# Performance work log

Measured on AMD Instinct MI355X. Metric: run time of the kernel, lower is better.

## Reference

```python
import jax, jax.numpy as jnp
import numpy as np

EPS = 1e-5
MODES = 64
KERNEL = 25
PRED = 336
N_ENC = 2

def rmsnorm(x, w):
    return x * jax.lax.rsqrt(jnp.mean(jnp.square(x), axis=-1, keepdims=True) + EPS) * w

def ffn(x, w1, b1, w2, b2):
    return jax.nn.gelu(x @ w1 + b1, approximate=False) @ w2 + b2

def series_decomp(x):
    # moving average with zero padding (Conv1d, kernel=KERNEL, weight=1/KERNEL)
    pad = (KERNEL - 1) // 2
    xp = jnp.pad(x, ((0, 0), (pad, pad), (0, 0)))
    cs = jnp.cumsum(xp, axis=1)
    cs = jnp.concatenate([jnp.zeros_like(cs[:, :1]), cs], axis=1)
    t = (cs[:, KERNEL:, :] - cs[:, :-KERNEL, :]) / KERNEL  # [B,T,C]
    return x - t, t

def fourier_block(x, w, nw):
    # x: [B,T,C]; w: [MODES,C,2] learned complex weights; nw: [C] rms scale
    B, T, C = x.shape
    Xf = jnp.fft.rfft(x, axis=1)                      # [B,F,C] complex64
    mag = jnp.sum(Xf[:, 1:].real**2 + Xf[:, 1:].imag**2, axis=-1)  # [B,F-1]
    K = min(MODES, Xf.shape[1] - 1)
    _, idx = jax.lax.top_k(mag, K)
    idx = idx + 1                                      # skip DC, [B,K]
    Xsel = jnp.take_along_axis(Xf, idx[:, :, None], axis=1)  # [B,K,C]
    Wc = w[:K, :, 0] + 1j * w[:K, :, 1]               # [K,C]
    Ysel = Xsel * Wc[None]                             # [B,K,C]
    Yf = jnp.zeros_like(Xf).at[jnp.arange(B)[:, None], idx].set(Ysel)
    y = jnp.fft.irfft(Yf, n=T, axis=1)                 # [B,T,C]
    return rmsnorm(y, nw)

def setup_inputs() -> dict:
    key = jax.random.key(0)
    ks = iter(jax.random.split(key, 64))
    B, L, Cin, Cout, D, FF = 32, 1024, 8, 8, 512, 2048
    r = lambda *s: jax.random.normal(next(ks), s, dtype=jnp.float32) * 0.02
    z = lambda *s: jnp.zeros(s, dtype=jnp.float32)
    o = lambda *s: jnp.ones(s, dtype=jnp.float32)
    return {
        'x': jax.random.normal(next(ks), (B, L, Cin), dtype=jnp.float32),
        'enc_in_w': r(Cin, D), 'enc_in_b': z(D),
        'dec_in_w': r(Cin, D), 'dec_in_b': z(D),
        'enc_freq_w': r(N_ENC, MODES, D, 2), 'enc_freq_nw': o(N_ENC, D),
        'enc_n1': o(N_ENC, D), 'enc_n2': o(N_ENC, D),
        'enc_w1': r(N_ENC, D, FF), 'enc_b1': z(N_ENC, FF),
        'enc_w2': r(N_ENC, FF, D), 'enc_b2': z(N_ENC, D),
        'dec_freq_w': r(MODES, D, 2), 'dec_freq_nw': o(D),
        'dec_n1': o(D), 'dec_n2': o(D), 'dec_nx': o(D),
        'dec_cross_w': r(D, D), 'dec_cross_b': z(D),
        'dec_w1': r(D, FF), 'dec_b1': z(FF),
        'dec_w2': r(FF, D), 'dec_b2': z(D),
        'seas_w': r(D, Cout), 'seas_b': z(Cout),
        'tr_w1': r(D, FF), 'tr_b1': z(FF),
        'tr_w2': r(FF, Cout), 'tr_b2': z(Cout),
        'mix_w': r(Cout, Cout), 'mix_b': z(Cout),
        'qpos': jax.random.normal(next(ks), (1, PRED, D), dtype=jnp.float32) * 0.02,
    }

def reference(x, enc_in_w, enc_in_b, dec_in_w, dec_in_b,
              enc_freq_w, enc_freq_nw, enc_n1, enc_n2, enc_w1, enc_b1, enc_w2, enc_b2,
              dec_freq_w, dec_freq_nw, dec_n1, dec_n2, dec_nx, dec_cross_w, dec_cross_b,
              dec_w1, dec_b1, dec_w2, dec_b2, seas_w, seas_b,
              tr_w1, tr_b1, tr_w2, tr_b2, mix_w, mix_b, qpos):
    s, t = series_decomp(x)
    sez = s @ enc_in_w + enc_in_b                      # [B,L,D]
    for i in range(N_ENC):
        sez = sez + fourier_block(rmsnorm(sez, enc_n1[i]), enc_freq_w[i], enc_freq_nw[i])
        sez = sez + ffn(rmsnorm(sez, enc_n2[i]), enc_w1[i], enc_b1[i], enc_w2[i], enc_b2[i])
    memory = sez
    tgt = qpos + sez[:, -1:, :]                        # [B,PRED,D]
    # decoder layer
    m = jnp.mean(memory, axis=1, keepdims=True)        # [B,1,D]
    m = rmsnorm(m, dec_nx) @ dec_cross_w + dec_cross_b
    y = fourier_block(rmsnorm(tgt, dec_n1), dec_freq_w, dec_freq_nw)
    xd = tgt + y * jax.nn.sigmoid(m)
    xd = xd + ffn(rmsnorm(xd, dec_n2), dec_w1, dec_b1, dec_w2, dec_b2)
    sez_out = xd @ seas_w + seas_b                     # [B,PRED,Cout]
    tr = t @ dec_in_w + dec_in_b
    tr_out = ffn(tr[:, -1:, :], tr_w1, tr_b1, tr_w2, tr_b2)  # [B,1,Cout], broadcasts
    out = sez_out + tr_out
    return out @ mix_w + mix_b
```

## Files before the change

### kernel.cpp

```cpp
#include <hip/hip_runtime.h>
#include <hip/hip_fp16.h>
#include <math.h>

#define B_    32
#define L_    1024
#define D_    512
#define FF_   2048
#define PRED_ 336
#define ME_   (B_*L_)
#define MD_   (B_*PRED_)
#define EPS_  1e-5f

typedef _Float16 f16;
typedef _Float16 f16x8 __attribute__((ext_vector_type(8)));
typedef float    f32x4 __attribute__((ext_vector_type(4)));

__device__ __forceinline__ float wred64(float v) {
#pragma unroll
  for (int o = 32; o > 0; o >>= 1) v += __shfl_xor(v, o, 64);
  return v;
}
__device__ __forceinline__ double dwred64(double v) {
#pragma unroll
  for (int o = 32; o > 0; o >>= 1) v += __shfl_xor(v, o, 64);
  return v;
}
__device__ __forceinline__ float gelu_f(float x) {
  return 0.5f * x * (1.0f + erff(x * 0.7071067811865476f));
}
__device__ __forceinline__ void gl2lds16(const void* g, void* l) {
  __builtin_amdgcn_global_load_lds((const __attribute__((address_space(1))) void*)g,
                                   (__attribute__((address_space(3))) void*)l, 16, 0, 0);
}

__global__ void k_transpose_cast(const float* __restrict__ in, f16* __restrict__ out, int R, int C) {
  __shared__ float t[32][33];
  int c0 = blockIdx.x * 32, r0 = blockIdx.y * 32;
  int tx = threadIdx.x, ty = threadIdx.y;
#pragma unroll
  for (int j = ty; j < 32; j += 8) t[j][tx] = in[(size_t)(r0 + j) * C + c0 + tx];
  __syncthreads();
#pragma unroll
  for (int j = ty; j < 32; j += 8) out[(size_t)(c0 + j) * R + r0 + tx] = (f16)t[tx][j];
}

__global__ __launch_bounds__(256) void k_decomp_proj(const float* __restrict__ x,
    const float* __restrict__ w, const float* __restrict__ bias, float* __restrict__ sez) {
  int b = blockIdx.x, t0 = blockIdx.y * 128, tid = threadIdx.x;
  __shared__ float xs[152][8];
  __shared__ float st[128][8];
  __shared__ float wsm[8 * 512];
  __shared__ float bs[512];
  for (int i = tid; i < 152 * 8; i += 256) {
    int tt = i >> 3, c = i & 7; int tg = t0 - 12 + tt;
    xs[tt][c] = (tg >= 0 && tg < 1024) ? x[((size_t)b * 1024 + tg) * 8 + c] : 0.0f;
  }
  for (int i = tid; i < 4096; i += 256) wsm[i] = w[i];
  for (int i = tid; i < 512; i += 256) bs[i] = bias[i];
  __syncthreads();
  for (int i = tid; i < 1024; i += 256) {
    int t = i >> 3, c = i & 7;
    float s = 0.f;
#pragma unroll
    for (int j = 0; j < 25; ++j) s += xs[t + j][c];
    st[t][c] = xs[t + 12][c] - s / 25.0f;
  }
  __syncthreads();
#pragma unroll
  for (int g = 0; g < 2; ++g) {
    int d = tid + g * 256;
    float wb[8];
#pragma unroll
    for (int c = 0; c < 8; ++c) wb[c] = wsm[c * 512 + d];
    float bb = bs[d];
    for (int t = 0; t < 128; ++t) {
      float o = bb;
#pragma unroll
      for (int c = 0; c < 8; ++c) o += st[t][c] * wb[c];
      sez[((size_t)b * 1024 + t0 + t) * 512 + d] = o;
    }
  }
}

__global__ __launch_bounds__(512) void k_trend_trin(const float* __restrict__ x, const float* __restrict__ w,
    const float* __restrict__ bias, float* __restrict__ trin) {
  int b = blockIdx.x, tid = threadIdx.x;
  __shared__ float tl[8];
  if (tid < 8) {
    float s = 0.f;
    for (int j = 1011; j <= 1023; ++j) s += x[((size_t)b * 1024 + j) * 8 + tid];
    tl[tid] = s / 25.0f;
  }
  __syncthreads();
  float acc = bias[tid];
#pragma unroll
  for (int c = 0; c < 8; ++c) acc += tl[c] * w[c * 512 + tid];
  trin[b * 512 + tid] = acc;
}

__global__ __launch_bounds__(256) void k_rinv(const float* __restrict__ xin, float* __restrict__ rinv) {
  int row = blockIdx.x * 4 + (threadIdx.x >> 6), lane = threadIdx.x & 63;
  const float4* p = (const float4*)(xin + (size_t)row * 512);
  float4 a = p[lane * 2], b = p[lane * 2 + 1];
  float ss = a.x*a.x + a.y*a.y + a.z*a.z + a.w*a.w + b.x*b.x + b.y*b.y + b.z*b.z + b.w*b.w;
  ss = wred64(ss);
  if (lane == 0) rinv[row] = rsqrtf(ss * (1.0f / 512.0f) + EPS_);
}

__global__ __launch_bounds__(256) void k_rms_f16(const float* __restrict__ xin, const float* __restrict__ w,
    f16* __restrict__ out) {
  int row = blockIdx.x * 4 + (threadIdx.x >> 6), lane = threadIdx.x & 63;
  const float4* p = (const float4*)(xin + (size_t)row * 512);
  float4 a = p[lane * 2], b = p[lane * 2 + 1];
  float ss = a.x*a.x + a.y*a.y + a.z*a.z + a.w*a.w + b.x*b.x + b.y*b.y + b.z*b.z + b.w*b.w;
  ss = wred64(ss);
  float ri = rsqrtf(ss * (1.0f / 512.0f) + EPS_);
  const float4* wp = (const float4*)w;
  float4 wa = wp[lane * 2], wb = wp[lane * 2 + 1];
  float va[8] = {a.x, a.y, a.z, a.w, b.x, b.y, b.z, b.w};
  float wv[8] = {wa.x, wa.y, wa.z, wa.w, wb.x, wb.y, wb.z, wb.w};
  f16x8 o;
#pragma unroll
  for (int j = 0; j < 8; ++j) o[j] = (f16)((va[j] * ri) * wv[j]);
  *(f16x8*)(out + (size_t)row * 512 + lane * 8) = o;
}

#define IDX_(i) ((i) + ((i) >> 4))
__global__ __launch_bounds__(256) void k_fft_enc(const float* __restrict__ sez, const float* __restrict__ rinv,
    const float* __restrict__ n1, float* __restrict__ Xf) {
  int b = blockIdx.x, c0 = blockIdx.y * 4, tid = threadIdx.x;
  __shared__ double Zr[2][1088], Zi[2][1088];
  __shared__ double TWr[256], TWi[256];
  if (tid < 256) {
    double a = -6.283185307179586232 * (double)tid / 1024.0;
    TWr[tid] = cos(a); TWi[tid] = sin(a);
  }
  for (int i = tid; i < 4096; i += 256) {
    int t = i >> 2, cl = i & 3;
    float xv = (sez[((size_t)b * 1024 + t) * 512 + c0 + cl] * rinv[b * 1024 + t]) * n1[c0 + cl];
    int u = t, rt = 0;
#pragma unroll
    for (int d = 0; d < 5; ++d) { rt = (rt << 2) | (u & 3); u >>= 2; }
    if (cl & 1) Zi[cl >> 1][IDX_(rt)] = (double)xv; else Zr[cl >> 1][IDX_(rt)] = (double)xv;
  }
  __syncthreads();
#pragma unroll
  for (int s = 0; s < 5; ++s) {
    const int lh = 2 * s, h = 1 << lh;
#pragma unroll
    for (int qi = 0; qi < 2; ++qi) {
      int q = tid + qi * 256;
      int p = q >> 8, qq = q & 255;
      int j = qq & (h - 1), g = qq >> lh;
      int p0 = (g << (lh + 2)) + j;
      int i0 = IDX_(p0), i1 = IDX_(p0 + h), i2 = IDX_(p0 + 2 * h), i3 = IDX_(p0 + 3 * h);
      int tw = j << (8 - lh);
      double w1r = TWr[tw], w1i = TWi[tw];
      double w2r = w1r * w1r - w1i * w1i, w2i = 2.0 * w1r * w1i;
      double w3r = w2r * w1r - w2i * w1i, w3i = w2r * w1i + w2i * w1r;
      double Ar = Zr[p][i0], Ai = Zi[p][i0];
      double br = Zr[p][i1], bi = Zi[p][i1];
      double cr = Zr[p][i2], ci = Zi[p][i2];
      double dr = Zr[p][i3], di = Zi[p][i3];
      double Br = br * w1r - bi * w1i, Bi = br * w1i + bi * w1r;
      double Cr = cr * w2r - ci * w2i, Ci = cr * w2i + ci * w2r;
      double Dr = dr * w3r - di * w3i, Di = dr * w3i + di * w3r;
      double T0r = Ar + Cr, T0i = Ai + Ci;
      double T1r = Ar - Cr, T1i = Ai - Ci;
      double T2r = Br + Dr, T2i = Bi + Di;
      double T3r = Bi - Di, T3i = Dr - Br;
      Zr[p][i0] = T0r + T2r; Zi[p][i0] = T0i + T2i;
      Zr[p][i1] = T1r + T3r; Zi[p][i1] = T1i + T3i;
      Zr[p][i2] = T0r - T2r; Zi[p][i2] = T0i - T2i;
      Zr[p][i3] = T1r - T3r; Zi[p][i3] = T1i - T3i;
    }
    __syncthreads();
  }
  for (int i = tid; i < 513 * 2; i += 256) {
    int f = i >> 1, p = i & 1;
    int mf = (1024 - f) & 1023;
    double Ar = Zr[p][IDX_(f)], Ai = Zi[p][IDX_(f)], Br = Zr[p][IDX_(mf)], Bi = Zi[p][IDX_(mf)];
    float4 o;
    o.x = (float)(0.5 * (Ar + Br)); o.y = (float)(0.5 * (Ai - Bi));
    o.z = (float)(0.5 * (Ai + Bi)); o.w = (float)(0.5 * (Br - Ar));
    *(float4*)&Xf[(((size_t)b * 513 + f) * 512 + c0 + 2 * p) * 2] = o;
  }
}

__global__ __launch_bounds__(256) void k_mag(const float* __restrict__ Xf, double* __restrict__ mag, int F) {
  int b = blockIdx.x, f = blockIdx.y + 1, tid = threadIdx.x;
  const float2* row = (const float2*)(Xf + ((size_t)b * F + f) * 512 * 2);
  double s = 0;
  for (int c = tid; c < 512; c += 256) { float2 v = row[c]; s += (double)v.x * v.x + (double)v.y * v.y; }
  s = dwred64(s);
  __shared__ double ps[4];
  if ((tid & 63) == 0) ps[tid >> 6] = s;
  __syncthreads();
  if (tid == 0) mag[b * 513 + f] = ps[0] + ps[1] + ps[2] + ps[3];
}

__global__ __launch_bounds__(256) void k_topk(const double* __restrict__ mag, int* __restrict__ idx, int F) {
  int b = blockIdx.x, tid = threadIdx.x;
  __shared__ double v[528];
  __shared__ double rv[256];
  __shared__ int ri[256];
  for (int s = tid; s < 528; s += 256) v[s] = (s >= 1 && s < F) ? mag[b * 513 + s] : -1e300;
  __syncthreads();
  for (int r = 0; r < 64; ++r) {
    double bv = -1e300; int bi = 0;
    for (int s = tid; s < 528; s += 256) { double xv = v[s]; if (xv > bv) { bv = xv; bi = s; } }
    rv[tid] = bv; ri[tid] = bi;
    __syncthreads();
    for (int st = 128; st > 0; st >>= 1) {
      if (tid < st) {
        double o = rv[tid + st]; int oi = ri[tid + st];
        if (o > rv[tid] || (o == rv[tid] && oi < ri[tid])) { rv[tid] = o; ri[tid] = oi; }
      }
      __syncthreads();
    }
    if (tid == 0) { idx[b * 64 + r] = ri[0]; v[ri[0]] = -1e300; }
    __syncthreads();
  }
}

__global__ __launch_bounds__(512) void k_gather(const float* __restrict__ Xf, const int* __restrict__ idx,
    const float* __restrict__ fw, float* __restrict__ Ysel, int F, int T) {
  int b = blockIdx.x, k = blockIdx.y, c = threadIdx.x;
  int f = idx[b * 64 + k];
  float sc = (2 * f == T) ? (1.0f / (float)T) : (2.0f / (float)T);
  float2 xv = *(const float2*)&Xf[(((size_t)b * F + f) * 512 + c) * 2];
  float wr = fw[(k * 512 + c) * 2], wi = fw[(k * 512 + c) * 2 + 1];
  float yr = (xv.x * wr - xv.y * wi) * sc;
  float yi = (xv.x * wi + xv.y * wr) * sc;
  *(float2*)&Ysel[((size_t)(b * 64 + k) * 512 + c) * 2] = make_float2(yr, yi);
}

template <int T>
__global__ __launch_bounds__(256) void k_irfft(const float* __restrict__ Ysel, const int* __restrict__ idx,
    const float* __restrict__ nw, const float* __restrict__ sig,
    float* __restrict__ dst, int mode) {
  int b = blockIdx.x, t0 = blockIdx.y * 16, tid = threadIdx.x;
  int cq = tid & 127;
  int tg = tid >> 7;
  __shared__ float tcT[16][68], tsT[16][68];
  __shared__ int sidx[64];
  __shared__ float red[4][8];
  __shared__ float rfac[16];
  if (tid < 64) sidx[tid] = idx[b * 64 + tid];
  __syncthreads();
  for (int i = tid; i < 1024; i += 256) {
    int k = i >> 4, tt = i & 15;
    int m = (sidx[k] * (t0 + tt)) % T;
    float ang = (float)m * (float)(6.283185307179586232 / (double)T);
    tcT[tt][k] = cosf(ang);
    tsT[tt][k] = sinf(ang);
  }
  __syncthreads();
  float acc[8][4];
#pragma unroll
  for (int q = 0; q < 8; ++q)
#pragma unroll
    for (int j = 0; j < 4; ++j) acc[q][j] = 0.f;
  const float4* ys = (const float4*)Ysel + (size_t)b * 64 * 256 + 2 * cq;
  for (int k4 = 0; k4 < 64; k4 += 4) {
    float4 ya[4], yb[4];
#pragma unroll
    for (int kk = 0; kk < 4; ++kk) {
      ya[kk] = ys[(size_t)(k4 + kk) * 256];
      yb[kk] = ys[(size_t)(k4 + kk) * 256 + 1];
    }
#pragma unroll
    for (int q = 0; q < 8; ++q) {
      int tt = tg * 8 + q;
      float4 c4 = *(const float4*)&tcT[tt][k4];
      float4 s4 = *(const float4*)&tsT[tt][k4];
      acc[q][0] += ya[0].x * c4.x - ya[0].y * s4.x;
      acc[q][1] += ya[0].z * c4.x - ya[0].w * s4.x;
      acc[q][2] += yb[0].x * c4.x - yb[0].y * s4.x;
      acc[q][3] += yb[0].z * c4.x - yb[0].w * s4.x;
      acc[q][0] += ya[1].x * c4.y - ya[1].y * s4.y;
      acc[q][1] += ya[1].z * c4.y - ya[1].w * s4.y;
      acc[q][2] += yb[1].x * c4.y - yb[1].y * s4.y;
      acc[q][3] += yb[1].z * c4.y - yb[1].w * s4.y;
      acc[q][0] += ya[2].x * c4.z - ya[2].y * s4.z;
      acc[q][1] += ya[2].z * c4.z - ya[2].w * s4.z;
      acc[q][2] += yb[2].x * c4.z - yb[2].y * s4.z;
      acc[q][3] += yb[2].z * c4.z - yb[2].w * s4.z;
      acc[q][0] += ya[3].x * c4.w - ya[3].y * s4.w;
      acc[q][1] += ya[3].z * c4.w - ya[3].w * s4.w;
      acc[q][2] += yb[3].x * c4.w - yb[3].y * s4.w;
      acc[q][3] += yb[3].z * c4.w - yb[3].w * s4.w;
    }
  }
  int lane = tid & 63, wv = tid >> 6;
#pragma unroll
  for (int q = 0; q < 8; ++q) {
    float v = wred64(acc[q][0] * acc[q][0] + acc[q][1] * acc[q][1]
                   + acc[q][2] * acc[q][2] + acc[q][3] * acc[q][3]);
    if (lane == 0) red[wv][q] = v;
  }
  __syncthreads();
  if (tid < 16) {
    int tg2 = tid >> 3, q = tid & 7;
    float s = red[tg2 * 2][q] + red[tg2 * 2 + 1][q];
    rfac[tid] = rsqrtf(s * (1.0f / 512.0f) + EPS_);
  }
  __syncthreads();
  int c = 4 * cq;
  float4 wc = *(const float4*)&nw[c];
  float4 sg = (mode == 1) ? *(const float4*)&sig[b * 512 + c] : make_float4(1.f, 1.f, 1.f, 1.f);
  float* drow = dst + ((size_t)b * T + t0) * 512 + c;
#pragma unroll
  for (int q = 0; q < 8; ++q) {
    int tt = tg * 8 + q;
    float rf = rfac[tt];
    float4 cur = *(float4*)&drow[(size_t)tt * 512];
    float y0 = (acc[q][0] * rf) * wc.x;
    float y1 = (acc[q][1] * rf) * wc.y;
    float y2 = (acc[q][2] * rf) * wc.z;
    float y3 = (acc[q][3] * rf) * wc.w;
    cur.x += (mode == 1) ? y0 * sg.x : y0;
    cur.y += (mode == 1) ? y1 * sg.y : y1;
    cur.z += (mode == 1) ? y2 * sg.z : y2;
    cur.w += (mode == 1) ? y3 * sg.w : y3;
    *(float4*)&drow[(size_t)tt * 512] = cur;
  }
}

template <int MODE>
__global__ __launch_bounds__(256) void k_gemm(const f16* __restrict__ A, const f16* __restrict__ Bt,
    const float* __restrict__ bias, float* __restrict__ Cf, f16* __restrict__ Ch,
    int M, int N, int K) {
  __shared__ f16 lA[2][128][64];
  __shared__ f16 lB[2][128][64];
  int bm = blockIdx.x, bn = blockIdx.y;
  int tid = threadIdx.x, lane = tid & 63, w = tid >> 6;
  int wr = w >> 1, wcq = w & 1;
  f32x4 acc[4][4];
#pragma unroll
  for (int i = 0; i < 4; ++i)
#pragma unroll
    for (int j = 0; j < 4; ++j) acc[i][j] = (f32x4){0.f, 0.f, 0.f, 0.f};
  int lr = lane >> 3;
  int kk = (lane & 7) * 8;
  int nk = K >> 6;
  auto STAGE = [&](int buf, int kt) {
#pragma unroll
    for (int i = 0; i < 4; ++i) {
      int rt = (w * 4 + i) * 8;
      int rr = rt + lr;
      gl2lds16(A + (size_t)(bm * 128 + rr) * K + kt * 64 + kk, &lA[buf][rt][0]);
      gl2lds16(Bt + (size_t)(bn * 128 + rr) * K + kt * 64 + kk, &lB[buf][rt][0]);
    }
  };
  STAGE(0, 0);
  int cur = 0;
  for (int kt = 0; kt < nk; ++kt) {
    if (kt + 1 < nk) {
      STAGE(cur ^ 1, kt + 1);
      asm volatile("s_waitcnt vmcnt(8)\n\ts_barrier" ::: "memory");
    } else {
      asm volatile("s_waitcnt vmcnt(0)\n\ts_barrier" ::: "memory");
    }
#pragma unroll
    for (int ki = 0; ki < 2; ++ki) {
      f16x8 af[4], bf[4];
#pragma unroll
      for (int mi = 0; mi < 4; ++mi)
        af[mi] = *(const f16x8*)&lA[cur][wr * 64 + mi * 16 + (lane & 15)][ki * 32 + (lane >> 4) * 8];
#pragma unroll
      for (int ni = 0; ni < 4; ++ni)
        bf[ni] = *(const f16x8*)&lB[cur][wcq * 64 + ni * 16 + (lane & 15)][ki * 32 + (lane >> 4) * 8];
#pragma unroll
      for (int mi = 0; mi < 4; ++mi)
#pragma unroll
        for (int ni = 0; ni < 4; ++ni)
          acc[mi][ni] = __builtin_amdgcn_mfma_f32_16x16x32_f16(af[mi], bf[ni], acc[mi][ni], 0, 0, 0);
    }
    asm volatile("s_barrier" ::: "memory");
    cur ^= 1;
  }
  int cbase = bn * 128 + wcq * 64;
  int rbase = bm * 128 + wr * 64;
#pragma unroll
  for (int mi = 0; mi < 4; ++mi)
#pragma unroll
    for (int ni = 0; ni < 4; ++ni) {
      int cg = cbase + ni * 16 + (lane & 15);
      float bv = bias[cg];
#pragma unroll
      for (int q = 0; q < 4; ++q) {
        int rg = rbase + mi * 16 + (lane >> 4) * 4 + q;
        float val = acc[mi][ni][q] + bv;
        if (MODE == 0) Ch[(size_t)rg * N + cg] = (f16)gelu_f(val);
        else           Cf[(size_t)rg * N + cg] += val;
      }
    }
}

__global__ __launch_bounds__(256) void k_mc_part(const float* __restrict__ sez, float* __restrict__ mcp) {
  int b = blockIdx.x, ch = blockIdx.y, tid = threadIdx.x;
  for (int d = tid; d < 512; d += 256) {
    float s = 0.f;
    for (int t = 0; t < 128; ++t) s += sez[((size_t)b * 1024 + ch * 128 + t) * 512 + d];
    mcp[((size_t)b * 8 + ch) * 512 + d] = s;
  }
}
__global__ __launch_bounds__(512) void k_mc_fin(const float* __restrict__ mcp, const float* __restrict__ nx,
    const float* __restrict__ Wc, const float* __restrict__ cb, float* __restrict__ sig) {
  int b = blockIdx.x, d = threadIdx.x;
  float m = 0.f;
#pragma unroll
  for (int ch = 0; ch < 8; ++ch) m += mcp[((size_t)b * 8 + ch) * 512 + d];
  m *= (1.0f / 1024.0f);
  float ss = wred64(m * m);
  __shared__ float ps[8];
  __shared__ float mn[512];
  int lane = d & 63, wv = d >> 6;
  if (lane == 0) ps[wv] = ss;
  __syncthreads();
  float tot = 0.f;
#pragma unroll
  for (int i = 0; i < 8; ++i) tot += ps[i];
  float ri = rsqrtf(tot * (1.0f / 512.0f) + EPS_);
  mn[d] = (m * ri) * nx[d];
  __syncthreads();
  float accv = cb[d];
  for (int e = 0; e < 512; ++e) accv += mn[e] * Wc[(size_t)e * 512 + d];
  sig[b * 512 + d] = 1.0f / (1.0f + expf(-accv));
}

__global__ __launch_bounds__(512) void k_make_tgt(const float* __restrict__ sez, const float* __restrict__ qpos,
    const float* __restrict__ n1, float* __restrict__ tgt, float* __restrict__ tgt_n,
    float* __restrict__ rinvd) {
  int row = blockIdx.x, d = threadIdx.x;
  int b = row / 336, p = row % 336;
  float v = qpos[(size_t)p * 512 + d] + sez[((size_t)b * 1024 + 1023) * 512 + d];
  tgt[(size_t)row * 512 + d] = v;
  float ss = wred64(v * v);
  __shared__ float ps[8];
  if ((d & 63) == 0) ps[d >> 6] = ss;
  __syncthreads();
  float t = 0.f;
#pragma unroll
  for (int i = 0; i < 8; ++i) t += ps[i];
  float ri = rsqrtf(t * (1.0f / 512.0f) + EPS_);
  tgt_n[(size_t)row * 512 + d] = (v * ri) * n1[d];
  if (d == 0) rinvd[row] = ri;
}

__global__ void k_dtab(double* __restrict__ dtt) {
  int f = blockIdx.x;
  for (int t = threadIdx.x; t < 336; t += 256) {
    double cv = 0.0, sv = 0.0;
    if (f < 169) {
      int m = (f * t) % 336;
      double a = 6.283185307179586232 * (double)m / 336.0;
      cv = cos(a); sv = sin(a);
    }
    dtt[((size_t)t * 176 + f) * 2]     = cv;
    dtt[((size_t)t * 176 + f) * 2 + 1] = sv;
  }
}
__global__ __launch_bounds__(512) void k_dft_dec(const float* __restrict__ tgt_n,
    const double* __restrict__ dtt, float* __restrict__ Xf) {
  int b = blockIdx.x, f0 = blockIdx.y * 4, c = threadIdx.x;
  double ar[4], ai[4];
#pragma unroll
  for (int i = 0; i < 4; ++i) { ar[i] = 0.0; ai[i] = 0.0; }
  const float* trow = tgt_n + (size_t)b * 336 * 512 + c;
  for (int t = 0; t < 336; ++t) {
    double xd = (double)trow[(size_t)t * 512];
    const double* tab = dtt + ((size_t)t * 176 + f0) * 2;
#pragma unroll
    for (int ff = 0; ff < 4; ++ff) {
      ar[ff] += xd * tab[ff * 2];
      ai[ff] -= xd * tab[ff * 2 + 1];
    }
  }
#pragma unroll
  for (int ff = 0; ff < 4; ++ff) {
    int f = f0 + ff;
    if (f < 169)
      *(float2*)&Xf[(((size_t)b * 169 + f) * 512 + c) * 2] = make_float2((float)ar[ff], (float)ai[ff]);
  }
}

__global__ __launch_bounds__(256) void k_tr_h(const float* __restrict__ trin, const float* __restrict__ w1,
    const float* __restrict__ b1, float* __restrict__ H) {
  int b = blockIdx.x, j0 = blockIdx.y * 512, tid = threadIdx.x;
  __shared__ float xs[512];
  for (int i = tid; i < 512; i += 256) xs[i] = trin[b * 512 + i];
  __syncthreads();
  int j = j0 + tid;
  float h0 = b1[j], h1 = b1[j + 256];
  const float* wp = w1 + j;
#pragma unroll 4
  for (int e = 0; e < 512; ++e) {
    float xe = xs[e];
    h0 += xe * wp[(size_t)e * 2048];
    h1 += xe * wp[(size_t)e * 2048 + 256];
  }
  H[b * 2048 + j] = gelu_f(h0);
  H[b * 2048 + j + 256] = gelu_f(h1);
}

__global__ __launch_bounds__(256) void k_tr_red(const float* __restrict__ H, const float* __restrict__ w2,
    const float* __restrict__ b2, float* __restrict__ trout) {
  int b = blockIdx.x, tid = threadIdx.x;
  __shared__ float red[4][8];
  float part[8];
#pragma unroll
  for (int co = 0; co < 8; ++co) part[co] = 0.f;
#pragma unroll
  for (int jj = 0; jj < 8; ++jj) {
    int j = tid + jj * 256;
    float g = H[b * 2048 + j];
    float4 wa = *(const float4*)&w2[(size_t)j * 8];
    float4 wb = *(const float4*)&w2[(size_t)j * 8 + 4];
    part[0] += g * wa.x; part[1] += g * wa.y; part[2] += g * wa.z; part[3] += g * wa.w;
    part[4] += g * wb.x; part[5] += g * wb.y; part[6] += g * wb.z; part[7] += g * wb.w;
  }
  int lane = tid & 63, wv = tid >> 6;
#pragma unroll
  for (int co = 0; co < 8; ++co) {
    float v = wred64(part[co]);
    if (lane == 0) red[wv][co] = v;
  }
  __syncthreads();
  if (tid < 8) trout[b * 8 + tid] = red[0][tid] + red[1][tid] + red[2][tid] + red[3][tid] + b2[tid];
}

__global__ __launch_bounds__(256) void k_head(const float* __restrict__ xd, const float* __restrict__ sw,
    const float* __restrict__ sb, const float* __restrict__ trout, const float* __restrict__ mw,
    const float* __restrict__ mb, float* __restrict__ outp) {
  int row = blockIdx.x, tid = threadIdx.x;
  int b = row / 336;
  __shared__ float wsm[512 * 8];
  __shared__ float red[4][8];
  __shared__ float srow[8];
  for (int i = tid; i < 4096; i += 256) wsm[i] = sw[i];
  __syncthreads();
  float part[8];
#pragma unroll
  for (int co = 0; co < 8; ++co) part[co] = 0.f;
#pragma unroll
  for (int g = 0; g < 2; ++g) {
    int d = tid + g * 256;
    float xv = xd[(size_t)row * 512 + d];
#pragma unroll
    for (int co = 0; co < 8; ++co) part[co] += xv * wsm[d * 8 + co];
  }
  int lane = tid & 63, wv = tid >> 6;
#pragma unroll
  for (int co = 0; co < 8; ++co) {
    float v = wred64(part[co]);
    if (lane == 0) red[wv][co] = v;
  }
  __syncthreads();
  if (tid == 0) {
#pragma unroll
    for (int co = 0; co < 8; ++co)
      srow[co] = red[0][co] + red[1][co] + red[2][co] + red[3][co] + sb[co] + trout[b * 8 + co];
  }
  __syncthreads();
  if (tid < 8) {
    float o = mb[tid];
#pragma unroll
    for (int co = 0; co < 8; ++co) o += srow[co] * mw[co * 8 + tid];
    outp[(size_t)row * 8 + tid] = o;
  }
}

extern "C" void kernel_launch(void* const* d_in, const int* in_sizes, int n_in,
                              void* d_out, int out_size, void* d_ws, size_t ws_size,
                              hipStream_t stream) {
  const float* x        = (const float*)d_in[0];
  const float* enc_in_w = (const float*)d_in[1];
  const float* enc_in_b = (const float*)d_in[2];
  const float* dec_in_w = (const float*)d_in[3];
  const float* dec_in_b = (const float*)d_in[4];
  const float* enc_fw   = (const float*)d_in[5];
  const float* enc_fnw  = (const float*)d_in[6];
  const float* enc_n1   = (const float*)d_in[7];
  const float* enc_n2   = (const float*)d_in[8];
  const float* enc_w1   = (const float*)d_in[9];
  const float* enc_b1   = (const float*)d_in[10];
  const float* enc_w2   = (const float*)d_in[11];
  const float* enc_b2   = (const float*)d_in[12];
  const float* dec_fw   = (const float*)d_in[13];
  const float* dec_fnw  = (const float*)d_in[14];
  const float* dec_n1   = (const float*)d_in[15];
  const float* dec_n2   = (const float*)d_in[16];
  const float* dec_nx   = (const float*)d_in[17];
  const float* dec_cw   = (const float*)d_in[18];
  const float* dec_cb   = (const float*)d_in[19];
  const float* dec_w1   = (const float*)d_in[20];
  const float* dec_b1   = (const float*)d_in[21];
  const float* dec_w2   = (const float*)d_in[22];
  const float* dec_b2   = (const float*)d_in[23];
  const float* seas_w   = (const float*)d_in[24];
  const float* seas_b   = (const float*)d_in[25];
  const float* tr_w1    = (const float*)d_in[26];
  const float* tr_b1    = (const float*)d_in[27];
  const float* tr_w2    = (const float*)d_in[28];
  const float* tr_b2    = (const float*)d_in[29];
  const float* mix_w    = (const float*)d_in[30];
  const float* mix_b    = (const float*)d_in[31];
  const float* qpos     = (const float*)d_in[32];
  float* outp = (float*)d_out;
  (void)in_sizes; (void)n_in; (void)out_size; (void)ws_size;

  char* wsb = (char*)d_ws;
  size_t off = 0;
  auto take = [&](size_t n) -> char* {
    char* p = wsb + off;
    off = (off + n + 255) & ~(size_t)255;
    return p;
  };
  float*  sez   = (float*)take((size_t)ME_ * 512 * 4);
  f16*    xn    = (f16*)take((size_t)ME_ * 512 * 2);
  const size_t XF_BYTES = (size_t)32 * 513 * 512 * 2 * 4;
  char*   arena = take(XF_BYTES + (size_t)32 * 64 * 512 * 2 * 4);
  float*  Xf    = (float*)arena;
  f16*    hbuf  = (f16*)arena;
  float*  Ysel  = (float*)(arena + XF_BYTES);
  float*  tgt   = (float*)take((size_t)MD_ * 512 * 4);
  float*  tgt_n = (float*)take((size_t)MD_ * 512 * 4);
  double* mag   = (double*)take((size_t)32 * 513 * 8);
  int*    idx   = (int*)take((size_t)32 * 64 * 4);
  float*  rinvp = (float*)take((size_t)ME_ * 4);
  float*  rinvd = (float*)take((size_t)MD_ * 4);
  float*  mcp   = (float*)take((size_t)32 * 8 * 512 * 4);
  float*  sig   = (float*)take((size_t)32 * 512 * 4);
  float*  trin  = (float*)take((size_t)32 * 512 * 4);
  float*  trout = (float*)take((size_t)32 * 8 * 4);
  float*  trH   = (float*)take((size_t)32 * 2048 * 4);
  double* dtt   = (double*)take((size_t)336 * 176 * 2 * 8);
  f16*    w1t   = (f16*)take((size_t)2 * 2048 * 512 * 2);
  f16*    w2t   = (f16*)take((size_t)2 * 512 * 2048 * 2);
  f16*    dw1t  = (f16*)take((size_t)2048 * 512 * 2);
  f16*    dw2t  = (f16*)take((size_t)512 * 2048 * 2);

  k_transpose_cast<<<dim3(64, 16), dim3(32, 8), 0, stream>>>(enc_w1, w1t, 512, 2048);
  k_transpose_cast<<<dim3(64, 16), dim3(32, 8), 0, stream>>>(enc_w1 + 512 * 2048, w1t + 2048 * 512, 512, 2048);
  k_transpose_cast<<<dim3(16, 64), dim3(32, 8), 0, stream>>>(enc_w2, w2t, 2048, 512);
  k_transpose_cast<<<dim3(16, 64), dim3(32, 8), 0, stream>>>(enc_w2 + 2048 * 512, w2t + 512 * 2048, 2048, 512);
  k_transpose_cast<<<dim3(64, 16), dim3(32, 8), 0, stream>>>(dec_w1, dw1t, 512, 2048);
  k_transpose_cast<<<dim3(16, 64), dim3(32, 8), 0, stream>>>(dec_w2, dw2t, 2048, 512);

  k_decomp_proj<<<dim3(32, 8), 256, 0, stream>>>(x, enc_in_w, enc_in_b, sez);
  k_trend_trin<<<32, 512, 0, stream>>>(x, dec_in_w, dec_in_b, trin);

  k_tr_h<<<dim3(32, 4), 256, 0, stream>>>(trin, tr_w1, tr_b1, trH);
  k_tr_red<<<32, 256, 0, stream>>>(trH, tr_w2, tr_b2, trout);

  for (int i = 0; i < 2; ++i) {
    k_rinv<<<ME_ / 4, 256, 0, stream>>>(sez, rinvp);
    k_fft_enc<<<dim3(32, 128), 256, 0, stream>>>(sez, rinvp, enc_n1 + i * 512, Xf);
    k_mag<<<dim3(32, 512), 256, 0, stream>>>(Xf, mag, 513);
    k_topk<<<32, 256, 0, stream>>>(mag, idx, 513);
    k_gather<<<dim3(32, 64), 512, 0, stream>>>(Xf, idx, enc_fw + (size_t)i * 64 * 512 * 2, Ysel, 513, 1024);
    k_irfft<1024><<<dim3(32, 64), 256, 0, stream>>>(Ysel, idx, enc_fnw + i * 512, nullptr, sez, 0);
    k_rms_f16<<<ME_ / 4, 256, 0, stream>>>(sez, enc_n2 + i * 512, xn);
    for (int ck = 0; ck < 2; ++ck) {
      const f16* Ax = xn + (size_t)ck * 16384 * 512;
      float* Cx = sez + (size_t)ck * 16384 * 512;
      k_gemm<0><<<dim3(128, 16), 256, 0, stream>>>(Ax, w1t + (size_t)i * 2048 * 512, enc_b1 + i * 2048,
                                                   nullptr, hbuf, 16384, 2048, 512);
      k_gemm<1><<<dim3(128, 4), 256, 0, stream>>>(hbuf, w2t + (size_t)i * 512 * 2048, enc_b2 + i * 512,
                                                  Cx, nullptr, 16384, 512, 2048);
    }
  }

  k_mc_part<<<dim3(32, 8), 256, 0, stream>>>(sez, mcp);
  k_mc_fin<<<32, 512, 0, stream>>>(mcp, dec_nx, dec_cw, dec_cb, sig);
  k_make_tgt<<<MD_, 512, 0, stream>>>(sez, qpos, dec_n1, tgt, tgt_n, rinvd);
  k_dtab<<<176, 256, 0, stream>>>(dtt);
  k_dft_dec<<<dim3(32, 43), 512, 0, stream>>>(tgt_n, dtt, Xf);
  k_mag<<<dim3(32, 168), 256, 0, stream>>>(Xf, mag, 169);
  k_topk<<<32, 256, 0, stream>>>(mag, idx, 169);
  k_gather<<<dim3(32, 64), 512, 0, stream>>>(Xf, idx, dec_fw, Ysel, 169, 336);
  k_irfft<336><<<dim3(32, 21), 256, 0, stream>>>(Ysel, idx, dec_fnw, sig, tgt, 1);
  k_rms_f16<<<MD_ / 4, 256, 0, stream>>>(tgt, dec_n2, xn);
  k_gemm<0><<<dim3(84, 16), 256, 0, stream>>>(xn, dw1t, dec_b1, nullptr, hbuf, MD_, 2048, 512);
  k_gemm<1><<<dim3(84, 4), 256, 0, stream>>>(hbuf, dw2t, dec_b2, tgt, nullptr, MD_, 512, 2048);

  k_head<<<MD_, 256, 0, stream>>>(tgt, seas_w, seas_b, trout, mix_w, mix_b, outp);
}
```

Baseline: 1.578 ms.

## Use single-wave register top-k and fp32 decoder DFT accumulation

The top-k kernel now runs as one 64-lane wavefront that holds the magnitudes in registers and does each argmax with shuffle reductions. This replaces the 256-thread shared-memory tree that needed about nine barriers per selected mode. Separately, the decoder DFT twiddle table and its accumulators switch from double to float, which cuts FP64 arithmetic and halves table traffic. The fp32 path may change which modes top-k picks when magnitudes are close.

```diff
diff --git a/kernel.cpp b/kernel.cpp
--- a/kernel.cpp
+++ b/kernel.cpp
@@ -199,27 +199,29 @@
   if (tid == 0) mag[b * 513 + f] = ps[0] + ps[1] + ps[2] + ps[3];
 }
 
-__global__ __launch_bounds__(256) void k_topk(const double* __restrict__ mag, int* __restrict__ idx, int F) {
-  int b = blockIdx.x, tid = threadIdx.x;
-  __shared__ double v[528];
-  __shared__ double rv[256];
-  __shared__ int ri[256];
-  for (int s = tid; s < 528; s += 256) v[s] = (s >= 1 && s < F) ? mag[b * 513 + s] : -1e300;
-  __syncthreads();
+__global__ __launch_bounds__(64) void k_topk(const double* __restrict__ mag, int* __restrict__ idx, int F) {
+  int b = blockIdx.x, lane = threadIdx.x;
+  double v[9];
+#pragma unroll
+  for (int j = 0; j < 9; ++j) {
+    int s = j * 64 + lane;
+    v[j] = (s >= 1 && s < F) ? mag[b * 513 + s] : -1e300;
+  }
   for (int r = 0; r < 64; ++r) {
     double bv = -1e300; int bi = 0;
-    for (int s = tid; s < 528; s += 256) { double xv = v[s]; if (xv > bv) { bv = xv; bi = s; } }
-    rv[tid] = bv; ri[tid] = bi;
-    __syncthreads();
-    for (int st = 128; st > 0; st >>= 1) {
-      if (tid < st) {
-        double o = rv[tid + st]; int oi = ri[tid + st];
-        if (o > rv[tid] || (o == rv[tid] && oi < ri[tid])) { rv[tid] = o; ri[tid] = oi; }
-      }
-      __syncthreads();
-    }
-    if (tid == 0) { idx[b * 64 + r] = ri[0]; v[ri[0]] = -1e300; }
-    __syncthreads();
+#pragma unroll
+    for (int j = 0; j < 9; ++j)
+      if (v[j] > bv) { bv = v[j]; bi = j * 64 + lane; }
+#pragma unroll
+    for (int o = 32; o > 0; o >>= 1) {
+      double ov = __shfl_xor(bv, o, 64);
+      int oi = __shfl_xor(bi, o, 64);
+      if (ov > bv || (ov == bv && oi < bi)) { bv = ov; bi = oi; }
+    }
+    if (lane == 0) idx[b * 64 + r] = bi;
+#pragma unroll
+    for (int j = 0; j < 9; ++j)
+      if (bi == j * 64 + lane) v[j] = -1e300;
   }
 }
 
@@ -449,40 +451,40 @@
   if (d == 0) rinvd[row] = ri;
 }
 
-__global__ void k_dtab(double* __restrict__ dtt) {
+__global__ void k_dtab(float* __restrict__ dtt) {
   int f = blockIdx.x;
   for (int t = threadIdx.x; t < 336; t += 256) {
-    double cv = 0.0, sv = 0.0;
+    float cv = 0.f, sv = 0.f;
     if (f < 169) {
       int m = (f * t) % 336;
       double a = 6.283185307179586232 * (double)m / 336.0;
-      cv = cos(a); sv = sin(a);
+      cv = (float)cos(a); sv = (float)sin(a);
     }
     dtt[((size_t)t * 176 + f) * 2]     = cv;
     dtt[((size_t)t * 176 + f) * 2 + 1] = sv;
   }
 }
 __global__ __launch_bounds__(512) void k_dft_dec(const float* __restrict__ tgt_n,
-    const double* __restrict__ dtt, float* __restrict__ Xf) {
+    const float* __restrict__ dtt, float* __restrict__ Xf) {
   int b = blockIdx.x, f0 = blockIdx.y * 4, c = threadIdx.x;
-  double ar[4], ai[4];
-#pragma unroll
-  for (int i = 0; i < 4; ++i) { ar[i] = 0.0; ai[i] = 0.0; }
+  float ar[4], ai[4];
+#pragma unroll
+  for (int i = 0; i < 4; ++i) { ar[i] = 0.f; ai[i] = 0.f; }
   const float* trow = tgt_n + (size_t)b * 336 * 512 + c;
   for (int t = 0; t < 336; ++t) {
-    double xd = (double)trow[(size_t)t * 512];
-    const double* tab = dtt + ((size_t)t * 176 + f0) * 2;
+    float xv = trow[(size_t)t * 512];
+    const float* tab = dtt + ((size_t)t * 176 + f0) * 2;
 #pragma unroll
     for (int ff = 0; ff < 4; ++ff) {
-      ar[ff] += xd * tab[ff * 2];
-      ai[ff] -= xd * tab[ff * 2 + 1];
+      ar[ff] += xv * tab[ff * 2];
+      ai[ff] -= xv * tab[ff * 2 + 1];
     }
   }
 #pragma unroll
   for (int ff = 0; ff < 4; ++ff) {
     int f = f0 + ff;
     if (f < 169)
-      *(float2*)&Xf[(((size_t)b * 169 + f) * 512 + c) * 2] = make_float2((float)ar[ff], (float)ai[ff]);
+      *(float2*)&Xf[(((size_t)b * 169 + f) * 512 + c) * 2] = make_float2(ar[ff], ai[ff]);
   }
 }
 
@@ -636,7 +638,7 @@
   float*  trin  = (float*)take((size_t)32 * 512 * 4);
   float*  trout = (float*)take((size_t)32 * 8 * 4);
   float*  trH   = (float*)take((size_t)32 * 2048 * 4);
-  double* dtt   = (double*)take((size_t)336 * 176 * 2 * 8);
+  float*  dtt   = (float*)take((size_t)336 * 176 * 2 * 4);
   f16*    w1t   = (f16*)take((size_t)2 * 2048 * 512 * 2);
   f16*    w2t   = (f16*)take((size_t)2 * 512 * 2048 * 2);
   f16*    dw1t  = (f16*)take((size_t)2048 * 512 * 2);
@@ -659,7 +661,7 @@
     k_rinv<<<ME_ / 4, 256, 0, stream>>>(sez, rinvp);
     k_fft_enc<<<dim3(32, 128), 256, 0, stream>>>(sez, rinvp, enc_n1 + i * 512, Xf);
     k_mag<<<dim3(32, 512), 256, 0, stream>>>(Xf, mag, 513);
-    k_topk<<<32, 256, 0, stream>>>(mag, idx, 513);
+    k_topk<<<32, 64, 0, stream>>>(mag, idx, 513);
     k_gather<<<dim3(32, 64), 512, 0, stream>>>(Xf, idx, enc_fw + (size_t)i * 64 * 512 * 2, Ysel, 513, 1024);
     k_irfft<1024><<<dim3(32, 64), 256, 0, stream>>>(Ysel, idx, enc_fnw + i * 512, nullptr, sez, 0);
     k_rms_f16<<<ME_ / 4, 256, 0, stream>>>(sez, enc_n2 + i * 512, xn);
@@ -679,7 +681,7 @@
   k_dtab<<<176, 256, 0, stream>>>(dtt);
   k_dft_dec<<<dim3(32, 43), 512, 0, stream>>>(tgt_n, dtt, Xf);
   k_mag<<<dim3(32, 168), 256, 0, stream>>>(Xf, mag, 169);
-  k_topk<<<32, 256, 0, stream>>>(mag, idx, 169);
+  k_topk<<<32, 64, 0, stream>>>(mag, idx, 169);
   k_gather<<<dim3(32, 64), 512, 0, stream>>>(Xf, idx, dec_fw, Ysel, 169, 336);
   k_irfft<336><<<dim3(32, 21), 256, 0, stream>>>(Ysel, idx, dec_fnw, sig, tgt, 1);
   k_rms_f16<<<MD_ / 4, 256, 0, stream>>>(tgt, dec_n2, xn);
```

Result: faster. 1.524 ms (-3.4%).
